# Performance work log

Measured on AMD Instinct MI355X. Metric: run time of the kernel, lower is better.

Reference implementation:

```python
import jax, jax.numpy as jnp
import numpy as np

NUM_HEAD = 16
EMB_DIM = 1024
HEAD_DIM = EMB_DIM // NUM_HEAD

def setup_inputs() -> dict:
    key = jax.random.key(0)
    ks = jax.random.split(key, 9)
    B, S, D = 2, 2048, EMB_DIM
    s = 1.0 / np.sqrt(D)
    return {
        "x": jax.random.normal(ks[0], (B, S, D), dtype=jnp.float32),
        "Wq": jax.random.normal(ks[1], (D, D), dtype=jnp.float32) * s,
        "bq": jnp.zeros((D,), dtype=jnp.float32),
        "Wk": jax.random.normal(ks[2], (D, D), dtype=jnp.float32) * s,
        "bk": jnp.zeros((D,), dtype=jnp.float32),
        "Wv": jax.random.normal(ks[3], (D, D), dtype=jnp.float32) * s,
        "bv": jnp.zeros((D,), dtype=jnp.float32),
        "Wo": jax.random.normal(ks[4], (D, D), dtype=jnp.float32) * s,
        "bo": jnp.zeros((D,), dtype=jnp.float32),
    }

def reference(x, Wq, bq, Wk, bk, Wv, bv, Wo, bo):
    B, S, D = x.shape
    H, Hd = NUM_HEAD, HEAD_DIM
    # projections (torch Linear: x @ W.T + b; here W stored as [in, out])
    Q = (x @ Wq + bq).reshape(B, S, H, Hd)
    K = (x @ Wk + bk).reshape(B, S, H, Hd)
    V = (x @ Wv + bv).reshape(B, S, H, Hd)
    scale = jnp.sqrt(jnp.asarray(Hd, dtype=x.dtype))
    scores = jnp.einsum('bqhd,bkhd->bhqk', Q, K) / scale  # [B,H,S,S]
    attn = jax.nn.softmax(scores, axis=-1)
    out = jnp.einsum('bhql,blhd->bqhd', attn, V).reshape(B, S, D)
    return out @ Wo + bo
```

## Files before the change

### kernel.cpp

```cpp
#include <hip/hip_runtime.h>
#include <math.h>


using bf16   = __bf16;
using bf16x8 = __attribute__((ext_vector_type(8))) __bf16;
using bf16x4 = __attribute__((ext_vector_type(4))) __bf16;
using f32x4  = __attribute__((ext_vector_type(4))) float;

#define MFMA16(a, b, c) __builtin_amdgcn_mfma_f32_16x16x32_bf16((a), (b), (c), 0, 0, 0)
#define WAIT_VM0() asm volatile("s_waitcnt vmcnt(0)" ::: "memory")
#define WAITBAR(N) asm volatile("s_waitcnt vmcnt(" #N ")\n\ts_barrier" ::: "memory")

__device__ __forceinline__ bf16x8 ld8(const bf16* p) { return *(const bf16x8*)p; }

__device__ __forceinline__ void ldg_lds16(bf16* lds_base, const bf16* g) {
    __builtin_amdgcn_global_load_lds(
        (const __attribute__((address_space(1))) void*)g,
        (__attribute__((address_space(3))) void*)lds_base, 16, 0, 0);
}

__device__ __forceinline__ float fast_exp2(float x) {
#if __has_builtin(__builtin_amdgcn_exp2f)
    return __builtin_amdgcn_exp2f(x);
#else
    return exp2f(x);
#endif
}

__global__ __launch_bounds__(256) void prep_kernel(
    const float* __restrict__ x, const float* __restrict__ Wq,
    const float* __restrict__ Wk, const float* __restrict__ Wv,
    const float* __restrict__ Wo, bf16* __restrict__ xb,
    bf16* __restrict__ WtBase) {
    const int z = blockIdx.z;
    const int tid = threadIdx.x;
    if (z == 4) {
        int id = blockIdx.y * 32 + blockIdx.x;
#pragma unroll
        for (int k = 0; k < 4; ++k) {
            int i = id * 4096 + k * 1024 + tid * 4;
            float4 v = *(const float4*)&x[i];
            bf16x4 o = { (bf16)v.x, (bf16)v.y, (bf16)v.z, (bf16)v.w };
            *(bf16x4*)&xb[i] = o;
        }
        return;
    }
    __shared__ float tile[32][33];
    const float* W = (z == 0) ? Wq : (z == 1) ? Wk : (z == 2) ? Wv : Wo;
    bf16* Wt = WtBase + (size_t)z * 1024 * 1024;
    const int tx = tid & 31, ty = tid >> 5;
    const int x0 = blockIdx.x * 32, y0 = blockIdx.y * 32;
#pragma unroll
    for (int i = 0; i < 4; ++i)
        tile[ty + i * 8][tx] = W[(size_t)(y0 + ty + i * 8) * 1024 + x0 + tx];
    __syncthreads();
#pragma unroll
    for (int i = 0; i < 4; ++i)
        Wt[(size_t)(x0 + ty + i * 8) * 1024 + y0 + tx] = (bf16)tile[tx][ty + i * 8];
}

__device__ __forceinline__ void gemm_stage(const bf16* __restrict__ src, int r0,
                                           int k0, bf16* dst, int w, int lane) {
#pragma unroll
    for (int c = 0; c < 2; ++c) {
        int flat = (w * 2 + c) * 64 + lane;
        int row = flat >> 2, cc = flat & 3;
        int gk = (cc ^ ((row >> 1) & 3)) * 8;
        ldg_lds16(dst + (size_t)(w * 2 + c) * 512,
                  src + (size_t)(r0 + row) * 1024 + k0 + gk);
    }
}

__device__ __forceinline__ void gemm_core_128(const bf16* __restrict__ A,
                                              const bf16* __restrict__ Bt,
                                              int m0, int n0,
                                              bf16* As, bf16* Bs,
                                              f32x4 (&acc)[4][4]) {
    const int tid = threadIdx.x, lane = tid & 63, w = tid >> 6;
    const int lo = lane & 15, quad = lane >> 4;
    const int wm = w >> 1, wn = w & 1;

    gemm_stage(A,  m0, 0, As, w, lane);
    gemm_stage(Bt, n0, 0, Bs, w, lane);
    WAIT_VM0();
    __syncthreads();

    for (int it = 0; it < 32; ++it) {
        const int buf = it & 1;
        if (it + 1 < 32) {
            gemm_stage(A,  m0, (it + 1) * 32, As + (buf ^ 1) * 4096, w, lane);
            gemm_stage(Bt, n0, (it + 1) * 32, Bs + (buf ^ 1) * 4096, w, lane);
        }
        const bf16* Ab = As + buf * 4096;
        const bf16* Bb = Bs + buf * 4096;
        bf16x8 af[4], bq[4];
#pragma unroll
        for (int t = 0; t < 4; ++t) {
            int r = wm * 64 + t * 16 + lo;
            af[t] = ld8(&Ab[r * 32 + ((quad ^ ((r >> 1) & 3)) * 8)]);
        }
#pragma unroll
        for (int t = 0; t < 4; ++t) {
            int r = wn * 64 + t * 16 + lo;
            bq[t] = ld8(&Bb[r * 32 + ((quad ^ ((r >> 1) & 3)) * 8)]);
        }
#pragma unroll
        for (int mt = 0; mt < 4; ++mt)
#pragma unroll
            for (int nt = 0; nt < 4; ++nt)
                acc[mt][nt] = MFMA16(af[mt], bq[nt], acc[mt][nt]);
        WAIT_VM0();
        __syncthreads();
    }
}

__global__ __launch_bounds__(256, 3) void qkv_gemm_kernel(
    const bf16* __restrict__ Xb, const bf16* __restrict__ Wts,
    const float* __restrict__ bq, const float* __restrict__ bk,
    const float* __restrict__ bv,
    bf16* __restrict__ Qo, bf16* __restrict__ Ko, bf16* __restrict__ Vto) {
    __shared__ bf16 Smem[4 * 4096];
    bf16* As = Smem;
    bf16* Bs = Smem + 2 * 4096;
    const int z = blockIdx.z;
    const bf16*  Bt   = Wts + (size_t)z * 1024 * 1024;
    const float* bias = (z == 0) ? bq : (z == 1) ? bk : bv;
    const int m0 = blockIdx.y * 128, n0 = blockIdx.x * 128;

    f32x4 acc[4][4] = {};
    gemm_core_128(Xb, Bt, m0, n0, As, Bs, acc);

    const int tid = threadIdx.x;
    const int lane = tid & 63, w = tid >> 6;
    const int lo = lane & 15, quad = lane >> 4;
    const int wm = w >> 1, wn = w & 1;
    const float QSCALE = 0.125f * 1.44269504088896f;

    if (z == 2) {
        bf16* T = Smem;
        const int b = m0 >> 11;
        const int s_base = m0 & 2047;
#pragma unroll
        for (int half = 0; half < 2; ++half) {
            __syncthreads();
            if (wm == half) {
#pragma unroll
                for (int nt = 0; nt < 4; ++nt)
#pragma unroll
                    for (int mt = 0; mt < 4; ++mt)
#pragma unroll
                        for (int r = 0; r < 4; ++r) {
                            int nn = wn * 64 + nt * 16 + lo;
                            int mm = mt * 16 + quad * 4 + r;
                            T[nn * 68 + mm] = (bf16)(acc[mt][nt][r] + bias[n0 + nn]);
                        }
            }
            __syncthreads();
#pragma unroll
            for (int p = 0; p < 8; ++p) {
                int pos = p * 1024 + tid * 4;
                int row = pos >> 6, col = pos & 63;
                int n = n0 + row, h = n >> 6, hd = n & 63;
                int colp = (col & 32) | (((col >> 2) & 3) << 3)
                         | (((col >> 4) & 1) << 2) | (col & 3);
                bf16x4 v = *(const bf16x4*)&T[row * 68 + col];
                *(bf16x4*)&Vto[((size_t)((b * 16 + h) * 64 + hd) << 11)
                               + s_base + half * 64 + colp] = v;
            }
        }
    } else {
#pragma unroll
        for (int mt = 0; mt < 4; ++mt)
#pragma unroll
            for (int nt = 0; nt < 4; ++nt)
#pragma unroll
                for (int r = 0; r < 4; ++r) {
                    int m = m0 + wm * 64 + mt * 16 + quad * 4 + r;
                    int n = n0 + wn * 64 + nt * 16 + lo;
                    float v = acc[mt][nt][r] + bias[n];
                    int b = m >> 11, s = m & 2047, h = n >> 6, hd = n & 63;
                    if (z == 0)
                        Qo[((size_t)((b * 16 + h) * 2048 + s) << 6) + hd] = (bf16)(v * QSCALE);
                    else
                        Ko[((size_t)((b * 16 + h) * 2048 + s) << 6) + hd] = (bf16)v;
                }
    }
}

__global__ __launch_bounds__(256, 2) void out_gemm_kernel(
    const bf16* __restrict__ A, const bf16* __restrict__ Bt,
    const float* __restrict__ bo, float* __restrict__ Co) {
    __shared__ bf16 As[2 * 2048];
    __shared__ bf16 Bs[2 * 4096];
    const int tid = threadIdx.x, lane = tid & 63, w = tid >> 6;
    const int lo = lane & 15, quad = lane >> 4;
    const int wm = w >> 1, wn = w & 1;
    const int m0 = blockIdx.y * 64, n0 = blockIdx.x * 128;

    auto stageA = [&](int k0, bf16* dst) {
        int flat = w * 64 + lane;
        int row = flat >> 2, cc = flat & 3;
        int gk = (cc ^ ((row >> 1) & 3)) * 8;
        ldg_lds16(dst + (size_t)w * 512, A + (size_t)(m0 + row) * 1024 + k0 + gk);
    };
    auto stageB = [&](int k0, bf16* dst) {
#pragma unroll
        for (int c = 0; c < 2; ++c) {
            int flat = (w * 2 + c) * 64 + lane;
            int row = flat >> 2, cc = flat & 3;
            int gk = (cc ^ ((row >> 1) & 3)) * 8;
            ldg_lds16(dst + (size_t)(w * 2 + c) * 512,
                      Bt + (size_t)(n0 + row) * 1024 + k0 + gk);
        }
    };

    f32x4 acc[2][4] = {};
    stageA(0, As);
    stageB(0, Bs);
    WAIT_VM0();
    __syncthreads();

    for (int it = 0; it < 32; ++it) {
        const int buf = it & 1;
        if (it + 1 < 32) {
            stageA((it + 1) * 32, As + (buf ^ 1) * 2048);
            stageB((it + 1) * 32, Bs + (buf ^ 1) * 4096);
        }
        const bf16* Ab = As + buf * 2048;
        const bf16* Bb = Bs + buf * 4096;
        bf16x8 af[2], bq[4];
#pragma unroll
        for (int t = 0; t < 2; ++t) {
            int r = wm * 32 + t * 16 + lo;
            af[t] = ld8(&Ab[r * 32 + ((quad ^ ((r >> 1) & 3)) * 8)]);
        }
#pragma unroll
        for (int t = 0; t < 4; ++t) {
            int r = wn * 64 + t * 16 + lo;
            bq[t] = ld8(&Bb[r * 32 + ((quad ^ ((r >> 1) & 3)) * 8)]);
        }
#pragma unroll
        for (int mt = 0; mt < 2; ++mt)
#pragma unroll
            for (int nt = 0; nt < 4; ++nt)
                acc[mt][nt] = MFMA16(af[mt], bq[nt], acc[mt][nt]);
        WAIT_VM0();
        __syncthreads();
    }

#pragma unroll
    for (int mt = 0; mt < 2; ++mt)
#pragma unroll
        for (int nt = 0; nt < 4; ++nt)
#pragma unroll
            for (int r = 0; r < 4; ++r) {
                int m = m0 + wm * 32 + mt * 16 + quad * 4 + r;
                int n = n0 + wn * 64 + nt * 16 + lo;
                Co[(size_t)m * 1024 + n] = acc[mt][nt][r] + bo[n];
            }
}

__global__ __launch_bounds__(256, 3) void attn_kernel(
    const bf16* __restrict__ Q, const bf16* __restrict__ K,
    const bf16* __restrict__ Vt, bf16* __restrict__ AO) {
    __shared__ bf16 Ks[3][64 * 64];
    __shared__ bf16 Vs[3][64 * 64];
    const int tid = threadIdx.x, w = tid >> 6, lane = tid & 63;
    const int lo = lane & 15, quad = lane >> 4;
    const int blk = blockIdx.x;
    const int bh = (blk & 7) | ((blk >> 7) << 3);
    const int qb = (blk >> 3) & 15;
    const int q0 = qb * 128 + w * 32;

    const bf16* Qb = Q + ((size_t)bh * 2048 + q0) * 64;
    const bf16* Kb = K + (size_t)bh * 2048 * 64;
    const bf16* Vb = Vt + (size_t)bh * 64 * 2048;

    bf16x8 qa[2][2];
#pragma unroll
    for (int qt = 0; qt < 2; ++qt)
#pragma unroll
        for (int ks = 0; ks < 2; ++ks)
            qa[qt][ks] = ld8(&Qb[(qt * 16 + lo) * 64 + ks * 32 + quad * 8]);

    f32x4 O[2][4] = {};
    float l_acc[2] = { 0.f, 0.f };

    auto stage = [&](int s0, int buf) {
#pragma unroll
        for (int c = 0; c < 2; ++c) {
            int flat = (w * 2 + c) * 64 + lane;
            int row = flat >> 3, cc = flat & 7;
            int g = (cc ^ (row & 7)) * 8;
            ldg_lds16(&Ks[buf][(w * 2 + c) * 512], &Kb[(size_t)(s0 + row) * 64 + g]);
            ldg_lds16(&Vs[buf][(w * 2 + c) * 512], &Vb[(size_t)row * 2048 + s0 + g]);
        }
    };

    const int swz = lo & 7;

    auto body = [&](int rbuf) {
        const bf16* Kt = &Ks[rbuf][0];
        const bf16* Vl = &Vs[rbuf][0];
        f32x4 S[2][4] = {};
#pragma unroll
        for (int t = 0; t < 4; ++t) {
            int r = t * 16 + lo;
#pragma unroll
            for (int ks = 0; ks < 2; ++ks) {
                bf16x8 kf = ld8(&Kt[r * 64 + (((quad + 4 * ks) ^ swz) * 8)]);
                S[0][t] = MFMA16(kf, qa[0][ks], S[0][t]);
                S[1][t] = MFMA16(kf, qa[1][ks], S[1][t]);
            }
        }
        bf16x8 pa[2][2];
#pragma unroll
        for (int qt = 0; qt < 2; ++qt)
#pragma unroll
            for (int kc = 0; kc < 2; ++kc) {
                float e0 = fast_exp2(S[qt][2 * kc][0]);
                float e1 = fast_exp2(S[qt][2 * kc][1]);
                float e2 = fast_exp2(S[qt][2 * kc][2]);
                float e3 = fast_exp2(S[qt][2 * kc][3]);
                float e4 = fast_exp2(S[qt][2 * kc + 1][0]);
                float e5 = fast_exp2(S[qt][2 * kc + 1][1]);
                float e6 = fast_exp2(S[qt][2 * kc + 1][2]);
                float e7 = fast_exp2(S[qt][2 * kc + 1][3]);
                l_acc[qt] += ((e0 + e1) + (e2 + e3)) + ((e4 + e5) + (e6 + e7));
                pa[qt][kc] = bf16x8{ (bf16)e0, (bf16)e1, (bf16)e2, (bf16)e3,
                                     (bf16)e4, (bf16)e5, (bf16)e6, (bf16)e7 };
            }
#pragma unroll
        for (int kc = 0; kc < 2; ++kc)
#pragma unroll
            for (int nt = 0; nt < 4; ++nt) {
                int r = nt * 16 + lo;
                bf16x8 vf = ld8(&Vl[r * 64 + ((((kc * 4 + quad) ^ swz)) * 8)]);
                O[0][nt] = MFMA16(pa[0][kc], vf, O[0][nt]);
                O[1][nt] = MFMA16(pa[1][kc], vf, O[1][nt]);
            }
    };

    stage(0, 0);
    stage(64, 1);
    WAITBAR(4);

    int rbuf = 0, sbuf = 2;
    for (int it = 0; it < 30; ++it) {
        stage((it + 2) * 64, sbuf);
        sbuf = (sbuf == 2) ? 0 : sbuf + 1;
        body(rbuf);
        WAITBAR(4);
        rbuf = (rbuf == 2) ? 0 : rbuf + 1;
    }
    body(rbuf);
    WAITBAR(0);
    rbuf = (rbuf == 2) ? 0 : rbuf + 1;
    body(rbuf);

    const int bb = bh >> 4, h = bh & 15;
#pragma unroll
    for (int qt = 0; qt < 2; ++qt) {
        float lt = l_acc[qt];
        lt += __shfl_xor(lt, 16, 64);
        lt += __shfl_xor(lt, 32, 64);
        const size_t outbase = ((size_t)(bb * 2048 + q0 + qt * 16)) * 1024 + h * 64;
#pragma unroll
        for (int r = 0; r < 4; ++r) {
            float rl = 1.0f / __shfl(lt, quad * 4 + r, 64);
            size_t rowoff = outbase + (size_t)(quad * 4 + r) * 1024;
#pragma unroll
            for (int nt = 0; nt < 4; ++nt)
                AO[rowoff + nt * 16 + lo] = (bf16)(O[qt][nt][r] * rl);
        }
    }
}

extern "C" void kernel_launch(void* const* d_in, const int* in_sizes, int n_in,
                              void* d_out, int out_size, void* d_ws, size_t ws_size,
                              hipStream_t stream) {
    const float* x  = (const float*)d_in[0];
    const float* Wq = (const float*)d_in[1];
    const float* bq = (const float*)d_in[2];
    const float* Wk = (const float*)d_in[3];
    const float* bk = (const float*)d_in[4];
    const float* Wv = (const float*)d_in[5];
    const float* bv = (const float*)d_in[6];
    const float* Wo = (const float*)d_in[7];
    const float* bo = (const float*)d_in[8];
    float* out = (float*)d_out;

    bf16* wsb = (bf16*)d_ws;
    const size_t M1 = 1024u * 1024u;
    bf16* Xb  = wsb;
    bf16* AO  = wsb;
    bf16* Wt  = wsb + 4 * M1;
    bf16* Qw  = wsb + 8 * M1;
    bf16* Kw  = wsb + 12 * M1;
    bf16* Vtw = wsb + 16 * M1;

    prep_kernel<<<dim3(32, 32, 5), 256, 0, stream>>>(x, Wq, Wk, Wv, Wo, Xb, Wt);
    qkv_gemm_kernel<<<dim3(8, 32, 3), 256, 0, stream>>>(Xb, Wt, bq, bk, bv, Qw, Kw, Vtw);
    attn_kernel<<<512, 256, 0, stream>>>(Qw, Kw, Vtw, AO);
    out_gemm_kernel<<<dim3(8, 64), 256, 0, stream>>>(AO, Wt + 3 * M1, bo, out);
}
```

Before: 181.7 us.

## Software-pipeline QK and PV across KV tiles with four-buffer LDS ring

```diff
diff --git a/kernel.cpp b/kernel.cpp
--- a/kernel.cpp
+++ b/kernel.cpp
@@ -260,11 +260,11 @@
             }
 }
 
-__global__ __launch_bounds__(256, 3) void attn_kernel(
+__global__ __launch_bounds__(256, 2) void attn_kernel(
     const bf16* __restrict__ Q, const bf16* __restrict__ K,
     const bf16* __restrict__ Vt, bf16* __restrict__ AO) {
-    __shared__ bf16 Ks[3][64 * 64];
-    __shared__ bf16 Vs[3][64 * 64];
+    __shared__ bf16 Ks[4][64 * 64];
+    __shared__ bf16 Vs[4][64 * 64];
     const int tid = threadIdx.x, w = tid >> 6, lane = tid & 63;
     const int lo = lane & 15, quad = lane >> 4;
     const int blk = blockIdx.x;
@@ -299,10 +299,13 @@
 
     const int swz = lo & 7;
 
-    auto body = [&](int rbuf) {
-        const bf16* Kt = &Ks[rbuf][0];
-        const bf16* Vl = &Vs[rbuf][0];
-        f32x4 S[2][4] = {};
+    auto qk = [&](int nb, f32x4 (&S)[2][4]) {
+        const bf16* Kt = &Ks[nb][0];
+#pragma unroll
+        for (int qt = 0; qt < 2; ++qt)
+#pragma unroll
+            for (int t = 0; t < 4; ++t)
+                S[qt][t] = f32x4{ 0.f, 0.f, 0.f, 0.f };
 #pragma unroll
         for (int t = 0; t < 4; ++t) {
             int r = t * 16 + lo;
@@ -313,23 +316,29 @@
                 S[1][t] = MFMA16(kf, qa[1][ks], S[1][t]);
             }
         }
-        bf16x8 pa[2][2];
+    };
+
+    auto expP = [&](f32x4 (&Sin)[2][4], bf16x8 (&pa)[2][2]) {
 #pragma unroll
         for (int qt = 0; qt < 2; ++qt)
 #pragma unroll
             for (int kc = 0; kc < 2; ++kc) {
-                float e0 = fast_exp2(S[qt][2 * kc][0]);
-                float e1 = fast_exp2(S[qt][2 * kc][1]);
-                float e2 = fast_exp2(S[qt][2 * kc][2]);
-                float e3 = fast_exp2(S[qt][2 * kc][3]);
-                float e4 = fast_exp2(S[qt][2 * kc + 1][0]);
-                float e5 = fast_exp2(S[qt][2 * kc + 1][1]);
-                float e6 = fast_exp2(S[qt][2 * kc + 1][2]);
-                float e7 = fast_exp2(S[qt][2 * kc + 1][3]);
+                float e0 = fast_exp2(Sin[qt][2 * kc][0]);
+                float e1 = fast_exp2(Sin[qt][2 * kc][1]);
+                float e2 = fast_exp2(Sin[qt][2 * kc][2]);
+                float e3 = fast_exp2(Sin[qt][2 * kc][3]);
+                float e4 = fast_exp2(Sin[qt][2 * kc + 1][0]);
+                float e5 = fast_exp2(Sin[qt][2 * kc + 1][1]);
+                float e6 = fast_exp2(Sin[qt][2 * kc + 1][2]);
+                float e7 = fast_exp2(Sin[qt][2 * kc + 1][3]);
                 l_acc[qt] += ((e0 + e1) + (e2 + e3)) + ((e4 + e5) + (e6 + e7));
                 pa[qt][kc] = bf16x8{ (bf16)e0, (bf16)e1, (bf16)e2, (bf16)e3,
                                      (bf16)e4, (bf16)e5, (bf16)e6, (bf16)e7 };
             }
+    };
+
+    auto pv = [&](int cb, bf16x8 (&pa)[2][2]) {
+        const bf16* Vl = &Vs[cb][0];
 #pragma unroll
         for (int kc = 0; kc < 2; ++kc)
 #pragma unroll
@@ -341,22 +350,35 @@
             }
     };
 
+    auto step = [&](f32x4 (&Sin)[2][4], f32x4 (&Sout)[2][4], int cb, int nb) {
+        bf16x8 pa[2][2];
+        expP(Sin, pa);
+        qk(nb, Sout);
+        pv(cb, pa);
+    };
+
     stage(0, 0);
     stage(64, 1);
     WAITBAR(4);
 
-    int rbuf = 0, sbuf = 2;
-    for (int it = 0; it < 30; ++it) {
-        stage((it + 2) * 64, sbuf);
-        sbuf = (sbuf == 2) ? 0 : sbuf + 1;
-        body(rbuf);
+    f32x4 Sa[2][4], Sb[2][4];
+    qk(0, Sa);
+
+    for (int it = 0; it < 30; it += 2) {
+        stage((it + 2) * 64, (it + 2) & 3);
         WAITBAR(4);
-        rbuf = (rbuf == 2) ? 0 : rbuf + 1;
-    }
-    body(rbuf);
+        step(Sa, Sb, it & 3, (it + 1) & 3);
+        stage((it + 3) * 64, (it + 3) & 3);
+        WAITBAR(4);
+        step(Sb, Sa, (it + 1) & 3, (it + 2) & 3);
+    }
     WAITBAR(0);
-    rbuf = (rbuf == 2) ? 0 : rbuf + 1;
-    body(rbuf);
+    step(Sa, Sb, 2, 3);
+    {
+        bf16x8 pa[2][2];
+        expP(Sb, pa);
+        pv(3, pa);
+    }
 
     const int bb = bh >> 4, h = bh & 15;
 #pragma unroll
```

Result: no change. 180.3 us (-0.8%).
